# Kernel tuning notes

Measured on AMD Instinct MI355X. Metric: run time of the kernel, lower is better.

The kernel has to match this reference:

```python
import jax, jax.numpy as jnp
import numpy as np

B, L, D = 4, 4096, 1024
S, H, DH = 256, 16, 64
TOPK = 8
NEG_INF = float('-inf')


def setup_inputs() -> dict:
    key = jax.random.key(0)
    ks = jax.random.split(key, 10)
    scale = 1.0 / np.sqrt(D)
    return {
        'token_states': jax.random.normal(ks[0], (B, L, D), dtype=jnp.float32),
        'Z_sets': jax.random.normal(ks[1], (B, S, H, DH), dtype=jnp.float32),
        'desc_q': jax.random.normal(ks[2], (B, S, D), dtype=jnp.float32),
        'mask_q': jnp.ones((B, S), dtype=bool),
        'Wg_w': jax.random.normal(ks[3], (D, D), dtype=jnp.float32) * scale,
        'Wg_b': jnp.zeros((D,), dtype=jnp.float32),
        'Wd_w': jax.random.normal(ks[4], (D, D), dtype=jnp.float32) * scale,
        'Wd_b': jnp.zeros((D,), dtype=jnp.float32),
        'out_w': jax.random.normal(ks[5], (D, D), dtype=jnp.float32) * scale,
        'out_b': jnp.zeros((D,), dtype=jnp.float32),
    }


def reference(token_states, Z_sets, desc_q, mask_q, Wg_w, Wg_b, Wd_w, Wd_b, out_w, out_b):
    # torch nn.Linear: y = x @ W.T + b
    Tproj = token_states @ Wg_w.T + Wg_b          # (B,L,D)
    Dproj = desc_q @ Wd_w.T + Wd_b                # (B,S,D)
    logits = jnp.einsum('bld,bsd->bls', Tproj, Dproj)  # (B,L,S)
    logits = jnp.where(mask_q[:, None, :], logits, NEG_INF)
    if TOPK > 0 and S > TOPK:
        vals, idx = jax.lax.top_k(logits, TOPK)   # (B,L,K)
        probs = jax.nn.softmax(vals, axis=-1)     # softmax over the K kept logits
        b_ix = jnp.arange(B)[:, None, None]
        l_ix = jnp.arange(L)[None, :, None]
        G = jnp.zeros_like(logits).at[b_ix, l_ix, idx].set(probs)
    else:
        G = jax.nn.softmax(logits, axis=-1)
    mix = jnp.einsum('bls,bshd->blhd', G, Z_sets)  # (B,L,H,DH)
    return mix.reshape(B, L, D) @ out_w.T + out_b
```

## Files before the change

### kernel.cpp

```cpp
#include <hip/hip_runtime.h>
#include <hip/hip_bf16.h>
#include <stdint.h>


#define B_ 4
#define L_ 4096
#define D_ 1024
#define S_ 256

typedef short s16x8 __attribute__((ext_vector_type(8)));
typedef _Float16 f16x8 __attribute__((ext_vector_type(8)));
typedef float f32x4 __attribute__((ext_vector_type(4)));

__device__ __forceinline__ unsigned short f2bf(float f) {
  uint32_t u = __float_as_uint(f);
  u += 0x7FFFu + ((u >> 16) & 1u);
  return (unsigned short)(u >> 16);
}
__device__ __forceinline__ float bf2f(unsigned short h) {
  return __uint_as_float(((uint32_t)h) << 16);
}
__device__ __forceinline__ unsigned short f2h(float f) {
  _Float16 h = (_Float16)f;
  return __builtin_bit_cast(unsigned short, h);
}
__device__ __forceinline__ int kperm32(int k5) {
  return (((k5 >> 2) & 3) << 3) | (((k5 >> 4) & 1) << 2) | (k5 & 3);
}

__global__ __launch_bounds__(256)
void prep_all(const float* __restrict__ desc, const float* __restrict__ Zf,
              const float* __restrict__ Wd, const float* __restrict__ oW,
              const float* __restrict__ Wg,
              unsigned short* __restrict__ dHi, unsigned short* __restrict__ dLo,
              unsigned short* __restrict__ zHi,
              unsigned short* __restrict__ wdHi, unsigned short* __restrict__ wdLo,
              unsigned short* __restrict__ owHi,
              unsigned short* __restrict__ wgTHi, unsigned short* __restrict__ wgTLo) {
  __shared__ float t[64][65];
  const int bid = blockIdx.x, tid = threadIdx.x;
  if (bid < 4096) {
    const float* src[4] = {desc, Zf, Wd, oW};
    unsigned short* hi[4] = {dHi, zHi, wdHi, owHi};
    unsigned short* lo[4] = {dLo, nullptr, wdLo, nullptr};
    int job = bid >> 10;
    int i = (bid & 1023) * 256 + tid;
    float4 v = reinterpret_cast<const float4*>(src[job])[i];
    int idx = i << 2;
    int nidx = (idx & ~31) | (((idx >> 2) & 3) << 3) | (((idx >> 4) & 1) << 2);
    float a[4] = {v.x, v.y, v.z, v.w};
    unsigned short hb[4];
#pragma unroll
    for (int e = 0; e < 4; ++e) hb[e] = f2bf(a[e]);
    *reinterpret_cast<ushort4*>(hi[job] + nidx) = make_ushort4(hb[0], hb[1], hb[2], hb[3]);
    if (lo[job]) {
      unsigned short lb[4];
#pragma unroll
      for (int e = 0; e < 4; ++e) lb[e] = f2bf(a[e] - bf2f(hb[e]));
      *reinterpret_cast<ushort4*>(lo[job] + nidx) = make_ushort4(lb[0], lb[1], lb[2], lb[3]);
    }
  } else {
    int tb = bid - 4096;
    int bx = tb & 15, by = tb >> 4;
    int c = tid & 63, r0 = tid >> 6;
#pragma unroll
    for (int rr = 0; rr < 16; ++rr) {
      int r = r0 * 16 + rr;
      t[r][c] = Wg[(size_t)(by * 64 + r) * 1024 + bx * 64 + c];
    }
    __syncthreads();
#pragma unroll
    for (int rr = 0; rr < 16; ++rr) {
      int r = r0 * 16 + rr;
      float v = t[c][r];
      int kcol = by * 64 + (c & 32) + kperm32(c & 31);
      size_t o = (size_t)(bx * 64 + r) * 1024 + kcol;
      unsigned short hb = f2bf(v);
      wgTHi[o] = hb;
      wgTLo[o] = f2bf(v - bf2f(hb));
    }
  }
}

__global__ __launch_bounds__(256, 2)
void gemm_a(const unsigned short* __restrict__ dHi, const unsigned short* __restrict__ dLo,
            const unsigned short* __restrict__ wdHi, const unsigned short* __restrict__ wdLo,
            const unsigned short* __restrict__ zHi, const unsigned short* __restrict__ owHi,
            float* __restrict__ P) {
  __shared__ unsigned short lAh[128 * 64], lAl[128 * 64];
  __shared__ unsigned short lBh[128 * 64], lBl[128 * 64];
  const int tid = threadIdx.x;
  const int w = tid >> 6, l = tid & 63;
  const int g = l >> 4, r15 = l & 15;
  const int rowBase = blockIdx.y * 128, colBase = blockIdx.x * 128;
  const int prob = blockIdx.z >> 2, kz = blockIdx.z & 3;
  const bool t3 = (prob == 0);
  const unsigned short* Ah = t3 ? dHi : zHi;
  const unsigned short* Bh = t3 ? wdHi : owHi;
  const int wr = (w >> 1) * 64, wc = (w & 1) * 64;
  const int k0 = kz * 256;

  f32x4 acc[4][4] = {};

  for (int kt = k0; kt < k0 + 256; kt += 64) {
    __syncthreads();
#pragma unroll
    for (int j = 0; j < 4; ++j) {
      int cl = j * 256 + tid;
      int r = cl >> 3;
      int c16 = (cl & 7) ^ (r & 7);
      long ao = (long)(rowBase + r) * 1024 + kt + c16 * 8;
      long bo = (long)(colBase + r) * 1024 + kt + c16 * 8;
      size_t doff = (size_t)(j * 256 + w * 64) * 8;
      __builtin_amdgcn_global_load_lds((const __attribute__((address_space(1))) void*)(Ah + ao),
                                       (__attribute__((address_space(3))) void*)(lAh + doff), 16, 0, 0);
      __builtin_amdgcn_global_load_lds((const __attribute__((address_space(1))) void*)(Bh + bo),
                                       (__attribute__((address_space(3))) void*)(lBh + doff), 16, 0, 0);
      if (t3) {
        __builtin_amdgcn_global_load_lds((const __attribute__((address_space(1))) void*)(dLo + ao),
                                         (__attribute__((address_space(3))) void*)(lAl + doff), 16, 0, 0);
        __builtin_amdgcn_global_load_lds((const __attribute__((address_space(1))) void*)(wdLo + bo),
                                         (__attribute__((address_space(3))) void*)(lBl + doff), 16, 0, 0);
      }
    }
    __syncthreads();
#pragma unroll
    for (int ks = 0; ks < 2; ++ks) {
      s16x8 ah[4], bh[4];
#pragma unroll
      for (int m = 0; m < 4; ++m) {
        int row = wr + m * 16 + r15;
        int offb = (row * 128 + ks * 64 + g * 16) ^ ((row & 7) << 4);
        ah[m] = *reinterpret_cast<const s16x8*>(reinterpret_cast<const char*>(lAh) + offb);
      }
#pragma unroll
      for (int n = 0; n < 4; ++n) {
        int row = wc + n * 16 + r15;
        int offb = (row * 128 + ks * 64 + g * 16) ^ ((row & 7) << 4);
        bh[n] = *reinterpret_cast<const s16x8*>(reinterpret_cast<const char*>(lBh) + offb);
      }
#pragma unroll
      for (int m = 0; m < 4; ++m)
#pragma unroll
        for (int n = 0; n < 4; ++n)
          acc[m][n] = __builtin_amdgcn_mfma_f32_16x16x32_bf16(ah[m], bh[n], acc[m][n], 0, 0, 0);
      if (t3) {
        s16x8 al[4], bl[4];
#pragma unroll
        for (int m = 0; m < 4; ++m) {
          int row = wr + m * 16 + r15;
          int offb = (row * 128 + ks * 64 + g * 16) ^ ((row & 7) << 4);
          al[m] = *reinterpret_cast<const s16x8*>(reinterpret_cast<const char*>(lAl) + offb);
        }
#pragma unroll
        for (int n = 0; n < 4; ++n) {
          int row = wc + n * 16 + r15;
          int offb = (row * 128 + ks * 64 + g * 16) ^ ((row & 7) << 4);
          bl[n] = *reinterpret_cast<const s16x8*>(reinterpret_cast<const char*>(lBl) + offb);
        }
#pragma unroll
        for (int m = 0; m < 4; ++m)
#pragma unroll
          for (int n = 0; n < 4; ++n) {
            acc[m][n] = __builtin_amdgcn_mfma_f32_16x16x32_bf16(al[m], bh[n], acc[m][n], 0, 0, 0);
            acc[m][n] = __builtin_amdgcn_mfma_f32_16x16x32_bf16(ah[m], bl[n], acc[m][n], 0, 0, 0);
          }
      }
    }
  }

  float* Cz = P + (long)blockIdx.z * (1 << 20);
#pragma unroll
  for (int m = 0; m < 4; ++m)
#pragma unroll
    for (int n = 0; n < 4; ++n) {
      int col = colBase + wc + n * 16 + r15;
#pragma unroll
      for (int q = 0; q < 4; ++q) {
        int row = rowBase + wr + m * 16 + g * 4 + q;
        Cz[(long)row * 1024 + col] = acc[m][n][q];
      }
    }
}

__global__ __launch_bounds__(256, 2)
void gemm_f3(const unsigned short* __restrict__ Ahi, const unsigned short* __restrict__ Alo,
             const unsigned short* __restrict__ Bhi, const unsigned short* __restrict__ Blo,
             float* __restrict__ C) {
  __shared__ unsigned short lAh[128 * 64], lAl[128 * 64];
  __shared__ unsigned short lBh[128 * 64], lBl[128 * 64];
  const int tid = threadIdx.x;
  const int w = tid >> 6, l = tid & 63;
  const int g = l >> 4, r15 = l & 15;
  const int rowBase = blockIdx.y * 128, colBase = blockIdx.x * 128;
  const int kz = blockIdx.z;
  const int wr = (w >> 1) * 64, wc = (w & 1) * 64;
  const int k0 = kz * 128;

  f32x4 acc[4][4] = {};

  for (int kt = k0; kt < k0 + 128; kt += 64) {
    __syncthreads();
#pragma unroll
    for (int j = 0; j < 4; ++j) {
      int cl = j * 256 + tid;
      int r = cl >> 3;
      int c16 = (cl & 7) ^ (r & 7);
      long ao = (long)(rowBase + r) * 1024 + kt + c16 * 8;
      long bo = (long)(colBase + r) * 1024 + kt + c16 * 8;
      size_t doff = (size_t)(j * 256 + w * 64) * 8;
      __builtin_amdgcn_global_load_lds((const __attribute__((address_space(1))) void*)(Ahi + ao),
                                       (__attribute__((address_space(3))) void*)(lAh + doff), 16, 0, 0);
      __builtin_amdgcn_global_load_lds((const __attribute__((address_space(1))) void*)(Alo + ao),
                                       (__attribute__((address_space(3))) void*)(lAl + doff), 16, 0, 0);
      __builtin_amdgcn_global_load_lds((const __attribute__((address_space(1))) void*)(Bhi + bo),
                                       (__attribute__((address_space(3))) void*)(lBh + doff), 16, 0, 0);
      __builtin_amdgcn_global_load_lds((const __attribute__((address_space(1))) void*)(Blo + bo),
                                       (__attribute__((address_space(3))) void*)(lBl + doff), 16, 0, 0);
    }
    __syncthreads();
#pragma unroll
    for (int ks = 0; ks < 2; ++ks) {
      s16x8 ah[4], al[4], bh[4], bl[4];
#pragma unroll
      for (int m = 0; m < 4; ++m) {
        int row = wr + m * 16 + r15;
        int offb = (row * 128 + ks * 64 + g * 16) ^ ((row & 7) << 4);
        ah[m] = *reinterpret_cast<const s16x8*>(reinterpret_cast<const char*>(lAh) + offb);
        al[m] = *reinterpret_cast<const s16x8*>(reinterpret_cast<const char*>(lAl) + offb);
      }
#pragma unroll
      for (int n = 0; n < 4; ++n) {
        int row = wc + n * 16 + r15;
        int offb = (row * 128 + ks * 64 + g * 16) ^ ((row & 7) << 4);
        bh[n] = *reinterpret_cast<const s16x8*>(reinterpret_cast<const char*>(lBh) + offb);
        bl[n] = *reinterpret_cast<const s16x8*>(reinterpret_cast<const char*>(lBl) + offb);
      }
#pragma unroll
      for (int m = 0; m < 4; ++m)
#pragma unroll
        for (int n = 0; n < 4; ++n) {
          acc[m][n] = __builtin_amdgcn_mfma_f32_16x16x32_bf16(ah[m], bh[n], acc[m][n], 0, 0, 0);
          acc[m][n] = __builtin_amdgcn_mfma_f32_16x16x32_bf16(al[m], bh[n], acc[m][n], 0, 0, 0);
          acc[m][n] = __builtin_amdgcn_mfma_f32_16x16x32_bf16(ah[m], bl[n], acc[m][n], 0, 0, 0);
        }
    }
  }

  float* Cz = C + (long)blockIdx.z * (1 << 20);
#pragma unroll
  for (int m = 0; m < 4; ++m)
#pragma unroll
    for (int n = 0; n < 4; ++n) {
      int col = colBase + wc + n * 16 + r15;
#pragma unroll
      for (int q = 0; q < 4; ++q) {
        int row = rowBase + wr + m * 16 + g * 4 + q;
        Cz[(long)row * 1024 + col] = acc[m][n][q];
      }
    }
}

__global__ __launch_bounds__(256)
void post_a(const float* __restrict__ P, const float* __restrict__ Wd_b,
            const float* __restrict__ out_b, const float* __restrict__ Wg_b,
            unsigned short* __restrict__ dpHi, unsigned short* __restrict__ dpLo,
            unsigned short* __restrict__ zwB, float* __restrict__ cb) {
  int w = threadIdx.x >> 6, l = threadIdx.x & 63;
  int job = blockIdx.x;
  if (job < 256) {
    int row = job * 4 + w;
    const float* r0 = P + (size_t)row * 1024;
    float s = 0.f;
#pragma unroll
    for (int j = 0; j < 4; ++j) {
      int i = j * 64 + l;
      float4 a0 = reinterpret_cast<const float4*>(r0)[i];
      float4 a1 = reinterpret_cast<const float4*>(r0 + (1 << 20))[i];
      float4 a2 = reinterpret_cast<const float4*>(r0 + 2 * (1 << 20))[i];
      float4 a3 = reinterpret_cast<const float4*>(r0 + 3 * (1 << 20))[i];
      float4 bb = reinterpret_cast<const float4*>(Wd_b)[i & 255];
      float4 v = make_float4(a0.x + a1.x + a2.x + a3.x + bb.x,
                             a0.y + a1.y + a2.y + a3.y + bb.y,
                             a0.z + a1.z + a2.z + a3.z + bb.z,
                             a0.w + a1.w + a2.w + a3.w + bb.w);
      float4 g = reinterpret_cast<const float4*>(Wg_b)[i & 255];
      s += v.x * g.x + v.y * g.y + v.z * g.z + v.w * g.w;
      int idx = i << 2;
      int nidx = (idx & ~31) | (((idx >> 2) & 3) << 3) | (((idx >> 4) & 1) << 2);
      float arr[4] = {v.x, v.y, v.z, v.w};
      unsigned short hb[4], lb[4];
#pragma unroll
      for (int e = 0; e < 4; ++e) {
        hb[e] = f2bf(arr[e]);
        lb[e] = f2bf(arr[e] - bf2f(hb[e]));
      }
      *reinterpret_cast<ushort4*>(dpHi + (size_t)row * 1024 + nidx) =
          make_ushort4(hb[0], hb[1], hb[2], hb[3]);
      *reinterpret_cast<ushort4*>(dpLo + (size_t)row * 1024 + nidx) =
          make_ushort4(lb[0], lb[1], lb[2], lb[3]);
    }
#pragma unroll
    for (int off = 32; off; off >>= 1) s += __shfl_xor(s, off);
    if (l == 0) cb[row] = s;
  } else {
    int row = (job - 256) * 4 + w;
    const float* r0 = P + 4 * (1 << 20) + (size_t)row * 1024;
#pragma unroll
    for (int j = 0; j < 4; ++j) {
      int i = j * 64 + l;
      float4 a0 = reinterpret_cast<const float4*>(r0)[i];
      float4 a1 = reinterpret_cast<const float4*>(r0 + (1 << 20))[i];
      float4 a2 = reinterpret_cast<const float4*>(r0 + 2 * (1 << 20))[i];
      float4 a3 = reinterpret_cast<const float4*>(r0 + 3 * (1 << 20))[i];
      float4 bb = reinterpret_cast<const float4*>(out_b)[i & 255];
      *reinterpret_cast<ushort4*>(zwB + (size_t)row * 1024 + (i << 2)) =
          make_ushort4(f2bf(a0.x + a1.x + a2.x + a3.x + bb.x),
                       f2bf(a0.y + a1.y + a2.y + a3.y + bb.y),
                       f2bf(a0.z + a1.z + a2.z + a3.z + bb.z),
                       f2bf(a0.w + a1.w + a2.w + a3.w + bb.w));
    }
  }
}

__global__ __launch_bounds__(256)
void post_mt(const float* __restrict__ P, unsigned short* __restrict__ mtF16) {
  int w = threadIdx.x >> 6, l = threadIdx.x & 63;
  int row = blockIdx.x * 4 + w;
  const float* r0 = P + (size_t)row * 1024;
#pragma unroll
  for (int j = 0; j < 4; ++j) {
    int i = j * 64 + l;
    float sx = 0.f, sy = 0.f, sz = 0.f, sw = 0.f;
#pragma unroll
    for (int p = 0; p < 8; ++p) {
      float4 a = reinterpret_cast<const float4*>(r0 + (size_t)p * (1 << 20))[i];
      sx += a.x; sy += a.y; sz += a.z; sw += a.w;
    }
    int idx = i << 2;
    int nidx = (idx & ~31) | (((idx >> 2) & 3) << 3) | (((idx >> 4) & 1) << 2);
    *reinterpret_cast<ushort4*>(mtF16 + (size_t)row * 1024 + nidx) =
        make_ushort4(f2h(sx), f2h(sy), f2h(sz), f2h(sw));
  }
}

__global__ __launch_bounds__(256, 2)
void gemm_topk(const float* __restrict__ A, const unsigned short* __restrict__ Bh16,
               const float* __restrict__ cb,
               int* __restrict__ tokIdx, float* __restrict__ tokP) {
  __shared__ unsigned short lA[32 * 64];
  __shared__ unsigned short lB[256 * 64];
  __shared__ float lgs[32][257];
  __shared__ float lcb[256];
  const int tid = threadIdx.x;
  const int w = tid >> 6, l = tid & 63;
  const int g = l >> 4, r15 = l & 15;
  int h = blockIdx.x;
  int lg = (h & 7) * 64 + (h >> 3);
  const int rowBase = lg * 32;
  const int batch = rowBase >> 12;
  const long zA = (long)rowBase * 1024;
  const long zB = (long)batch * (256 * 1024);
  lcb[tid] = cb[batch * 256 + tid];

  f32x4 acc[2][4] = {};

  for (int kt = 0; kt < 1024; kt += 64) {
    float4 av[2];
#pragma unroll
    for (int j = 0; j < 2; ++j) {
      int cl = j * 256 + tid;
      int r = cl >> 4, k4 = cl & 15;
      av[j] = *reinterpret_cast<const float4*>(A + zA + (long)r * 1024 + kt + k4 * 4);
    }
    __syncthreads();
#pragma unroll
    for (int j = 0; j < 8; ++j) {
      int cl = j * 256 + tid;
      int r = cl >> 3;
      int c16 = (cl & 7) ^ (r & 7);
      long bo = zB + (long)r * 1024 + kt + c16 * 8;
      size_t doff = (size_t)(j * 256 + w * 64) * 8;
      __builtin_amdgcn_global_load_lds((const __attribute__((address_space(1))) void*)(Bh16 + bo),
                                       (__attribute__((address_space(3))) void*)(lB + doff), 16, 0, 0);
    }
#pragma unroll
    for (int j = 0; j < 2; ++j) {
      int cl = j * 256 + tid;
      int r = cl >> 4, k4 = cl & 15;
      int byteoff = r * 128 + ((k4 >> 3) << 6) + ((k4 & 3) << 4) + (((k4 >> 2) & 1) << 3);
      int swz = byteoff ^ ((r & 7) << 4);
      *reinterpret_cast<ushort4*>(reinterpret_cast<char*>(lA) + swz) =
          make_ushort4(f2h(av[j].x), f2h(av[j].y), f2h(av[j].z), f2h(av[j].w));
    }
    __syncthreads();
#pragma unroll
    for (int ks = 0; ks < 2; ++ks) {
      f16x8 ah[2], bh[4];
#pragma unroll
      for (int m = 0; m < 2; ++m) {
        int row = m * 16 + r15;
        int offb = (row * 128 + ks * 64 + g * 16) ^ ((row & 7) << 4);
        ah[m] = *reinterpret_cast<const f16x8*>(reinterpret_cast<const char*>(lA) + offb);
      }
#pragma unroll
      for (int n = 0; n < 4; ++n) {
        int row = w * 64 + n * 16 + r15;
        int offb = (row * 128 + ks * 64 + g * 16) ^ ((row & 7) << 4);
        bh[n] = *reinterpret_cast<const f16x8*>(reinterpret_cast<const char*>(lB) + offb);
      }
#pragma unroll
      for (int m = 0; m < 2; ++m)
#pragma unroll
        for (int n = 0; n < 4; ++n)
          acc[m][n] = __builtin_amdgcn_mfma_f32_16x16x32_f16(ah[m], bh[n], acc[m][n], 0, 0, 0);
    }
  }

  __syncthreads();
#pragma unroll
  for (int m = 0; m < 2; ++m)
#pragma unroll
    for (int n = 0; n < 4; ++n) {
      int col = w * 64 + n * 16 + r15;
#pragma unroll
      for (int q = 0; q < 4; ++q) {
        int rloc = m * 16 + g * 4 + q;
        lgs[rloc][col] = acc[m][n][q] + lcb[col];
      }
    }
  __syncthreads();

  if (tid < 32) {
    int row = tid;
    uint32_t v0 = 0, v1 = 0, v2 = 0, v3 = 0, v4 = 0, v5 = 0, v6 = 0, v7 = 0;
    for (int s0 = 0; s0 < 256; s0 += 8) {
#pragma unroll
      for (int u = 0; u < 8; ++u) {
        float val = lgs[row][s0 + u];
        uint32_t iu = __float_as_uint(val);
        uint32_t x = (iu ^ ((uint32_t)((int)iu >> 31) | 0x80000000u));
        x = (x & 0xFFFFFF00u) | (uint32_t)(255 - (s0 + u));
        uint32_t w0 = (x > v1) ? v1 : (x > v0 ? x : v0);
        uint32_t w1 = (x > v2) ? v2 : (x > v1 ? x : v1);
        uint32_t w2 = (x > v3) ? v3 : (x > v2 ? x : v2);
        uint32_t w3 = (x > v4) ? v4 : (x > v3 ? x : v3);
        uint32_t w4 = (x > v5) ? v5 : (x > v4 ? x : v4);
        uint32_t w5 = (x > v6) ? v6 : (x > v5 ? x : v5);
        uint32_t w6 = (x > v7) ? v7 : (x > v6 ? x : v6);
        uint32_t w7 = (x > v7) ? x : v7;
        v0 = w0; v1 = w1; v2 = w2; v3 = w3; v4 = w4; v5 = w5; v6 = w6; v7 = w7;
      }
    }
    uint32_t keys[8] = {v0, v1, v2, v3, v4, v5, v6, v7};
    float vals[8];
    int sidx[8];
#pragma unroll
    for (int i = 0; i < 8; ++i) {
      int s = 255 - (int)(keys[i] & 255u);
      sidx[i] = s;
      vals[i] = lgs[row][s];
    }
    float m = vals[0];
#pragma unroll
    for (int i = 1; i < 8; ++i) m = fmaxf(m, vals[i]);
    float p[8], ssum = 0.f;
#pragma unroll
    for (int i = 0; i < 8; ++i) { p[i] = __expf(vals[i] - m); ssum += p[i]; }
    float inv = 1.f / ssum;
    long t = rowBase + row;
#pragma unroll
    for (int i = 0; i < 8; ++i) {
      tokIdx[t * 8 + i] = batch * 256 + sidx[i];
      tokP[t * 8 + i] = p[i] * inv;
    }
  }
}

__global__ __launch_bounds__(256)
void mix_k(const int* __restrict__ tokIdx, const float* __restrict__ tokP,
           const unsigned short* __restrict__ zwB, float* __restrict__ out) {
  int w = threadIdx.x >> 6, l = threadIdx.x & 63;
  long t = (long)blockIdx.x * 4 + w;
  int ridx[8];
  float wt[8];
#pragma unroll
  for (int i = 0; i < 8; ++i) {
    ridx[i] = tokIdx[t * 8 + i];
    wt[i] = tokP[t * 8 + i];
  }
  float acc[16] = {};
#pragma unroll
  for (int i = 0; i < 8; ++i) {
    const unsigned short* zr = zwB + (long)ridx[i] * 1024 + l * 16;
    uint4 q0 = *reinterpret_cast<const uint4*>(zr);
    uint4 q1 = *reinterpret_cast<const uint4*>(zr + 8);
    uint32_t qs[8] = {q0.x, q0.y, q0.z, q0.w, q1.x, q1.y, q1.z, q1.w};
#pragma unroll
    for (int e = 0; e < 8; ++e) {
      acc[e * 2]     += wt[i] * __uint_as_float(qs[e] << 16);
      acc[e * 2 + 1] += wt[i] * __uint_as_float(qs[e] & 0xFFFF0000u);
    }
  }
  float* orow = out + t * 1024 + l * 16;
#pragma unroll
  for (int j = 0; j < 4; ++j)
    reinterpret_cast<float4*>(orow)[j] =
        make_float4(acc[j * 4], acc[j * 4 + 1], acc[j * 4 + 2], acc[j * 4 + 3]);
}

extern "C" void kernel_launch(void* const* d_in, const int* in_sizes, int n_in,
                              void* d_out, int out_size, void* d_ws, size_t ws_size,
                              hipStream_t stream) {
  const float* token = (const float*)d_in[0];
  const float* Z     = (const float*)d_in[1];
  const float* descq = (const float*)d_in[2];
  const float* Wg    = (const float*)d_in[4];
  const float* Wg_b  = (const float*)d_in[5];
  const float* Wd    = (const float*)d_in[6];
  const float* Wd_b  = (const float*)d_in[7];
  const float* outW  = (const float*)d_in[8];
  const float* out_b = (const float*)d_in[9];
  float* out = (float*)d_out;
  (void)in_sizes; (void)n_in; (void)out_size; (void)ws_size;

  char* ws = (char*)d_ws;
  const size_t MB = 1u << 20;
  unsigned short* dHi   = (unsigned short*)(ws + 0 * MB);
  unsigned short* dLo   = (unsigned short*)(ws + 2 * MB);
  unsigned short* wdHi  = (unsigned short*)(ws + 4 * MB);
  unsigned short* wdLo  = (unsigned short*)(ws + 6 * MB);
  unsigned short* zHi   = (unsigned short*)(ws + 8 * MB);
  unsigned short* owHi  = (unsigned short*)(ws + 10 * MB);
  unsigned short* wgTHi = (unsigned short*)(ws + 12 * MB);
  unsigned short* wgTLo = (unsigned short*)(ws + 14 * MB);
  float*          P     = (float*)         (ws + 16 * MB);
  unsigned short* dpHi  = (unsigned short*)(ws + 0 * MB);
  unsigned short* dpLo  = (unsigned short*)(ws + 2 * MB);
  unsigned short* mtF16 = (unsigned short*)(ws + 4 * MB);
  unsigned short* zwB   = (unsigned short*)(ws + 8 * MB);
  float*          cb    = (float*)         (ws + 10 * MB);
  int*            tokIdx= (int*)           (ws + 10 * MB + 512 * 1024);
  float*          tokP  = (float*)         (ws + 11 * MB);

  prep_all<<<4352, 256, 0, stream>>>(descq, Z, Wd, outW, Wg,
                                     dHi, dLo, zHi, wdHi, wdLo, owHi,
                                     wgTHi, wgTLo);

  gemm_a<<<dim3(8, 8, 8), 256, 0, stream>>>(dHi, dLo, wdHi, wdLo, zHi, owHi, P);

  post_a<<<512, 256, 0, stream>>>(P, Wd_b, out_b, Wg_b, dpHi, dpLo, zwB, cb);

  gemm_f3<<<dim3(8, 8, 8), 256, 0, stream>>>(dpHi, dpLo, wgTHi, wgTLo, P);

  post_mt<<<256, 256, 0, stream>>>(P, mtF16);

  gemm_topk<<<512, 256, 0, stream>>>(token, mtF16, cb, tokIdx, tokP);

  mix_k<<<4096, 256, 0, stream>>>(tokIdx, tokP, zwB, out);
}
```

Before: 115.8 us.

## Load GEMM fragments directly from global and parallelize top-k selection across threads

The logits GEMM in gemm_topk stops staging A and B tiles through LDS. Each wave now loads its MFMA fragments straight from global memory, converting A from fp32 to fp16 in registers, which removes the per-k-step barriers and LDS traffic. The top-k scan also becomes two stages: all 256 threads each take 32 columns of a row and keep a local top-8, then 32 threads merge 64 candidates per row instead of scanning 256 serially. The cost is that fragments shared across waves are no longer reused from LDS, so global and L2 traffic rises and the loads are less coalesced.

Measured after the change: 147.5 us. +27.4%, slower.

```diff
diff --git a/kernel.cpp b/kernel.cpp
--- a/kernel.cpp
+++ b/kernel.cpp
@@ -348,9 +348,8 @@
 void gemm_topk(const float* __restrict__ A, const unsigned short* __restrict__ Bh16,
                const float* __restrict__ cb,
                int* __restrict__ tokIdx, float* __restrict__ tokP) {
-  __shared__ unsigned short lA[32 * 64];
-  __shared__ unsigned short lB[256 * 64];
   __shared__ float lgs[32][257];
+  __shared__ uint32_t lkeys[32][65];
   __shared__ float lcb[256];
   const int tid = threadIdx.x;
   const int w = tid >> 6, l = tid & 63;
@@ -366,48 +365,23 @@
   f32x4 acc[2][4] = {};
 
   for (int kt = 0; kt < 1024; kt += 64) {
-    float4 av[2];
-#pragma unroll
-    for (int j = 0; j < 2; ++j) {
-      int cl = j * 256 + tid;
-      int r = cl >> 4, k4 = cl & 15;
-      av[j] = *reinterpret_cast<const float4*>(A + zA + (long)r * 1024 + kt + k4 * 4);
-    }
-    __syncthreads();
-#pragma unroll
-    for (int j = 0; j < 8; ++j) {
-      int cl = j * 256 + tid;
-      int r = cl >> 3;
-      int c16 = (cl & 7) ^ (r & 7);
-      long bo = zB + (long)r * 1024 + kt + c16 * 8;
-      size_t doff = (size_t)(j * 256 + w * 64) * 8;
-      __builtin_amdgcn_global_load_lds((const __attribute__((address_space(1))) void*)(Bh16 + bo),
-                                       (__attribute__((address_space(3))) void*)(lB + doff), 16, 0, 0);
-    }
-#pragma unroll
-    for (int j = 0; j < 2; ++j) {
-      int cl = j * 256 + tid;
-      int r = cl >> 4, k4 = cl & 15;
-      int byteoff = r * 128 + ((k4 >> 3) << 6) + ((k4 & 3) << 4) + (((k4 >> 2) & 1) << 3);
-      int swz = byteoff ^ ((r & 7) << 4);
-      *reinterpret_cast<ushort4*>(reinterpret_cast<char*>(lA) + swz) =
-          make_ushort4(f2h(av[j].x), f2h(av[j].y), f2h(av[j].z), f2h(av[j].w));
-    }
-    __syncthreads();
 #pragma unroll
     for (int ks = 0; ks < 2; ++ks) {
       f16x8 ah[2], bh[4];
 #pragma unroll
       for (int m = 0; m < 2; ++m) {
-        int row = m * 16 + r15;
-        int offb = (row * 128 + ks * 64 + g * 16) ^ ((row & 7) << 4);
-        ah[m] = *reinterpret_cast<const f16x8*>(reinterpret_cast<const char*>(lA) + offb);
+        const float* ap = A + zA + (long)(m * 16 + r15) * 1024 + kt + ks * 32 + 4 * g;
+        float4 q0 = *reinterpret_cast<const float4*>(ap);
+        float4 q1 = *reinterpret_cast<const float4*>(ap + 16);
+        ah[m][0] = (_Float16)q0.x; ah[m][1] = (_Float16)q0.y;
+        ah[m][2] = (_Float16)q0.z; ah[m][3] = (_Float16)q0.w;
+        ah[m][4] = (_Float16)q1.x; ah[m][5] = (_Float16)q1.y;
+        ah[m][6] = (_Float16)q1.z; ah[m][7] = (_Float16)q1.w;
       }
 #pragma unroll
       for (int n = 0; n < 4; ++n) {
-        int row = w * 64 + n * 16 + r15;
-        int offb = (row * 128 + ks * 64 + g * 16) ^ ((row & 7) << 4);
-        bh[n] = *reinterpret_cast<const f16x8*>(reinterpret_cast<const char*>(lB) + offb);
+        long bo = zB + (long)(w * 64 + n * 16 + r15) * 1024 + kt + ks * 32 + 8 * g;
+        bh[n] = *reinterpret_cast<const f16x8*>(Bh16 + bo);
       }
 #pragma unroll
       for (int m = 0; m < 2; ++m)
@@ -417,7 +391,6 @@
     }
   }
 
-  __syncthreads();
 #pragma unroll
   for (int m = 0; m < 2; ++m)
 #pragma unroll
@@ -431,26 +404,47 @@
     }
   __syncthreads();
 
+  {
+    int row = tid >> 3, seg = tid & 7;
+    uint32_t v0 = 0, v1 = 0, v2 = 0, v3 = 0, v4 = 0, v5 = 0, v6 = 0, v7 = 0;
+#pragma unroll
+    for (int u = 0; u < 32; ++u) {
+      int s = seg * 32 + u;
+      float val = lgs[row][s];
+      uint32_t iu = __float_as_uint(val);
+      uint32_t x = (iu ^ ((uint32_t)((int)iu >> 31) | 0x80000000u));
+      x = (x & 0xFFFFFF00u) | (uint32_t)(255 - s);
+      uint32_t w0 = (x > v1) ? v1 : (x > v0 ? x : v0);
+      uint32_t w1 = (x > v2) ? v2 : (x > v1 ? x : v1);
+      uint32_t w2 = (x > v3) ? v3 : (x > v2 ? x : v2);
+      uint32_t w3 = (x > v4) ? v4 : (x > v3 ? x : v3);
+      uint32_t w4 = (x > v5) ? v5 : (x > v4 ? x : v4);
+      uint32_t w5 = (x > v6) ? v6 : (x > v5 ? x : v5);
+      uint32_t w6 = (x > v7) ? v7 : (x > v6 ? x : v6);
+      uint32_t w7 = (x > v7) ? x : v7;
+      v0 = w0; v1 = w1; v2 = w2; v3 = w3; v4 = w4; v5 = w5; v6 = w6; v7 = w7;
+    }
+    uint32_t ks8[8] = {v0, v1, v2, v3, v4, v5, v6, v7};
+#pragma unroll
+    for (int i = 0; i < 8; ++i) lkeys[row][seg * 8 + i] = ks8[i];
+  }
+  __syncthreads();
+
   if (tid < 32) {
     int row = tid;
     uint32_t v0 = 0, v1 = 0, v2 = 0, v3 = 0, v4 = 0, v5 = 0, v6 = 0, v7 = 0;
-    for (int s0 = 0; s0 < 256; s0 += 8) {
-#pragma unroll
-      for (int u = 0; u < 8; ++u) {
-        float val = lgs[row][s0 + u];
-        uint32_t iu = __float_as_uint(val);
-        uint32_t x = (iu ^ ((uint32_t)((int)iu >> 31) | 0x80000000u));
-        x = (x & 0xFFFFFF00u) | (uint32_t)(255 - (s0 + u));
-        uint32_t w0 = (x > v1) ? v1 : (x > v0 ? x : v0);
-        uint32_t w1 = (x > v2) ? v2 : (x > v1 ? x : v1);
-        uint32_t w2 = (x > v3) ? v3 : (x > v2 ? x : v2);
-        uint32_t w3 = (x > v4) ? v4 : (x > v3 ? x : v3);
-        uint32_t w4 = (x > v5) ? v5 : (x > v4 ? x : v4);
-        uint32_t w5 = (x > v6) ? v6 : (x > v5 ? x : v5);
-        uint32_t w6 = (x > v7) ? v7 : (x > v6 ? x : v6);
-        uint32_t w7 = (x > v7) ? x : v7;
-        v0 = w0; v1 = w1; v2 = w2; v3 = w3; v4 = w4; v5 = w5; v6 = w6; v7 = w7;
-      }
+#pragma unroll
+    for (int j = 0; j < 64; ++j) {
+      uint32_t x = lkeys[row][j];
+      uint32_t w0 = (x > v1) ? v1 : (x > v0 ? x : v0);
+      uint32_t w1 = (x > v2) ? v2 : (x > v1 ? x : v1);
+      uint32_t w2 = (x > v3) ? v3 : (x > v2 ? x : v2);
+      uint32_t w3 = (x > v4) ? v4 : (x > v3 ? x : v3);
+      uint32_t w4 = (x > v5) ? v5 : (x > v4 ? x : v4);
+      uint32_t w5 = (x > v6) ? v6 : (x > v5 ? x : v5);
+      uint32_t w6 = (x > v7) ? v7 : (x > v6 ? x : v6);
+      uint32_t w7 = (x > v7) ? x : v7;
+      v0 = w0; v1 = w1; v2 = w2; v3 = w3; v4 = w4; v5 = w5; v6 = w6; v7 = w7;
     }
     uint32_t keys[8] = {v0, v1, v2, v3, v4, v5, v6, v7};
     float vals[8];
```
